# Kernel optimization log

Measured on AMD Instinct MI355X. Metric: run time of the kernel, lower is better.

## Reference

```python
import jax, jax.numpy as jnp
import numpy as np

N_NODES = 10000
N_EDGES = 100000
D_IN = 2 * 1280   # concat of row/col node embeddings
H1 = 512
H2 = 256


def gcn_conv(x, edge_index, W, b):
    """PyG GCNConv: add self-loops, symmetric deg^-1/2 normalization,
    x @ W then scatter-add of normalized messages, plus bias.
    num_nodes is inferred from x.shape[0] (here = n_edges, faithful to source)."""
    N = x.shape[0]
    loops = jnp.arange(N, dtype=edge_index.dtype)
    row = jnp.concatenate([edge_index[0], loops])  # sources
    col = jnp.concatenate([edge_index[1], loops])  # targets
    deg = jax.ops.segment_sum(jnp.ones_like(row, dtype=x.dtype), col, num_segments=N)
    dinv = jax.lax.rsqrt(deg)  # deg >= 1 thanks to self-loops
    norm = dinv[row] * dinv[col]  # [E+N]
    h = x @ W  # [N, out]
    out = jax.ops.segment_sum(h[row] * norm[:, None], col, num_segments=N)
    return out + b


def setup_inputs() -> dict:
    key = jax.random.key(0)
    ks = jax.random.split(key, 9)
    x = jax.random.normal(ks[0], (N_NODES, 1280), dtype=jnp.float32)
    edge_index = jax.random.randint(ks[1], (2, N_EDGES), 0, N_NODES, dtype=jnp.int32)
    # uniform noise for gumbel-sigmoid (torch.rand); keep strictly in (0,1)
    eps = jax.random.uniform(ks[2], (N_EDGES, 1), jnp.float32, 1e-6, 1.0 - 1e-6)
    W1 = jax.random.normal(ks[3], (D_IN, H1), jnp.float32) * (1.0 / np.sqrt(D_IN))
    b1 = jnp.zeros((H1,), jnp.float32)
    W2 = jax.random.normal(ks[4], (H1, H2), jnp.float32) * (1.0 / np.sqrt(H1))
    b2 = jnp.zeros((H2,), jnp.float32)
    Wl = jax.random.normal(ks[5], (H2, 1), jnp.float32) * (1.0 / np.sqrt(H2))
    bl = jnp.zeros((1,), jnp.float32)
    return {"x": x, "edge_index": edge_index, "eps": eps,
            "W1": W1, "b1": b1, "W2": W2, "b2": b2, "Wl": Wl, "bl": bl}


def reference(x, edge_index, eps, W1, b1, W2, b2, Wl, bl):
    rows, cols = edge_index[0], edge_index[1]
    # per-edge explainer input: concat of endpoint embeddings -> [E, 2560]
    input_embs = jnp.concatenate([x[rows], x[cols]], axis=1)
    h = jax.nn.relu(gcn_conv(input_embs, edge_index, W1, b1))
    h = jax.nn.relu(gcn_conv(h, edge_index, W2, b2))
    pre = h @ Wl + bl  # [E, 1] sampling weights
    # gumbel-sigmoid sampling (temperature = 1.0)
    gate = jnp.log(eps) - jnp.log1p(-eps) + pre
    mask = jax.nn.sigmoid(gate)
    pos, neg = mask, 1.0 - mask
    kld = jnp.mean(pos * jnp.log(pos / 0.5 + 1e-8) + neg * jnp.log(neg / 0.5 + 1e-9))
    return (kld, mask)
```

## Files before the change

kernel.cpp:

```cpp
#include <hip/hip_runtime.h>
#include <cstdint>
#include <cstddef>

#define H1DIM 512
#define H2DIM 256
#define DNODE 1280
#define NPACK 1024
#define APAD  40

typedef __attribute__((ext_vector_type(8))) short short8v;
typedef __attribute__((ext_vector_type(4))) float f32x4;
typedef __attribute__((ext_vector_type(4))) unsigned short us4;

__device__ __forceinline__ unsigned short f2bf(float f) {
    unsigned int u = __builtin_bit_cast(unsigned int, f);
    u += 0x7fffu + ((u >> 16) & 1u);
    return (unsigned short)(u >> 16);
}
__device__ __forceinline__ float bf2f(unsigned short h) {
    unsigned int u = ((unsigned int)h) << 16;
    return __builtin_bit_cast(float, u);
}

__global__ void hist_k(const int* __restrict__ e1, int* __restrict__ hist, int E) {
    int e = blockIdx.x * 256 + threadIdx.x;
    if (e < E) atomicAdd(&hist[e1[e]], 1);
}
__global__ __launch_bounds__(1024) void scan_dinv_k(
    const int* __restrict__ hist, int* __restrict__ off, int* __restrict__ cursor,
    float* __restrict__ dinv, int N)
{
    __shared__ int part[1024];
    const int t = threadIdx.x;
    const int per = (N + 1023) / 1024;
    const int base = t * per;
    int s = 0;
    for (int i = 0; i < per; ++i) { int b = base + i; if (b < N) s += hist[b]; }
    part[t] = s;
    __syncthreads();
    for (int d = 1; d < 1024; d <<= 1) {
        int v = (t >= d) ? part[t - d] : 0;
        __syncthreads();
        part[t] += v;
        __syncthreads();
    }
    int run = (t == 0) ? 0 : part[t - 1];
    for (int i = 0; i < per; ++i) {
        int b = base + i;
        if (b < N) {
            int h = hist[b];
            off[b] = run;
            run += h;
            cursor[b] = 0;
            dinv[b] = rsqrtf(1.0f + (float)h);
        }
    }
    if (t == 1023) off[N] = run;
}
__global__ void fill_k(const int* __restrict__ e0, const int* __restrict__ e1,
                       const int* __restrict__ off, int* __restrict__ cursor,
                       int* __restrict__ srcs, int E) {
    int e = blockIdx.x * 256 + threadIdx.x;
    if (e < E) {
        int t = e1[e];
        int p = off[t] + atomicAdd(&cursor[t], 1);
        srcs[p] = e0[e];
    }
}

__global__ void cvt_x_k(const float* __restrict__ src, unsigned short* __restrict__ dst, int n) {
    int i = blockIdx.x * 256 + threadIdx.x;
    if (i * 4 < n) {
        f32x4 v = *reinterpret_cast<const f32x4*>(src + (size_t)i * 4);
        us4 o;
        o[0] = f2bf(v.x); o[1] = f2bf(v.y); o[2] = f2bf(v.z); o[3] = f2bf(v.w);
        *reinterpret_cast<us4*>(dst + (size_t)i * 4) = o;
    }
}

__global__ __launch_bounds__(256) void transpose_cvt_k(
    const float* __restrict__ src, unsigned short* __restrict__ dst, int ldsrc, int lddst)
{
    __shared__ float tile[32][33];
    const int c0 = blockIdx.x * 32;
    const int r0 = blockIdx.y * 32;
    const int tx = threadIdx.x & 31;
    const int ty = threadIdx.x >> 5;
#pragma unroll
    for (int rr = ty; rr < 32; rr += 8)
        tile[rr][tx] = src[(size_t)(r0 + rr) * ldsrc + c0 + tx];
    __syncthreads();
#pragma unroll
    for (int rr = ty; rr < 32; rr += 8)
        dst[(size_t)(c0 + rr) * lddst + r0 + tx] = f2bf(tile[tx][rr]);
}

template <int MODE>
__global__ __launch_bounds__(512) void gemm_u_k(
    const unsigned short* __restrict__ Ab,
    const unsigned short* __restrict__ Bt,
    unsigned short* __restrict__ Cb,
    const unsigned short* __restrict__ out1b,
    const unsigned short* __restrict__ XWb16,
    const float* __restrict__ b1,
    const float* __restrict__ b2,
    const float* __restrict__ Wl,
    const int* __restrict__ e0, const int* __restrict__ e1,
    float* __restrict__ h2f, float* __restrict__ pre_raw,
    int M, int K, int Nn, int nwg)
{
    __shared__ unsigned short As[2][128 * APAD];
    __shared__ unsigned short Bs[2][256 * APAD];
    __shared__ float b1s[H1DIM];
    __shared__ float b2s[H2DIM];
    __shared__ float wls[H2DIM];
    __shared__ float preacc[128];

    const int tid  = threadIdx.x;
    const int lane = tid & 63;
    const int w    = tid >> 6;
    const int wm   = w >> 2, wn = w & 3;

    int mb, n0;
    if (MODE == 0) {
        const int q = nwg >> 3, r = nwg & 7;
        const int xcd = blockIdx.x & 7;
        const int base = (xcd < r) ? xcd * (q + 1) : r * (q + 1) + (xcd - r) * q;
        const int wg = base + (blockIdx.x >> 3);
        mb = wg >> 2;
        n0 = (wg & 3) << 8;
    } else {
        mb = blockIdx.x;
        n0 = 0;
    }
    const int m0 = mb * 128;

    if (MODE == 1) {
        if (tid < 128) preacc[tid] = 0.f;
        if (tid < 256) { b2s[tid] = b2[tid]; wls[tid] = Wl[tid]; }
        b1s[tid] = b1[tid];
    }

    const int sa_r = tid >> 2, sa_k = (tid & 3) << 3;
    const int sb_r = tid >> 1, sb_k = (tid & 1) << 4;
    const int gma  = m0 + sa_r;
    const bool aval = (gma < M);

    const unsigned short* bsrc = Bt + (size_t)(n0 + sb_r) * K + sb_k;
    const unsigned short* s1 = nullptr;
    const unsigned short* s2 = nullptr;
    bool dual = false;
    if (MODE == 0) {
        if (aval) s1 = Ab + (size_t)gma * K + sa_k;
    } else if (aval) {
        if (gma < Nn) {
            s1 = out1b + (size_t)gma * H1DIM + sa_k;
        } else {
            s1 = XWb16 + (size_t)e0[gma] * NPACK + sa_k;
            s2 = XWb16 + (size_t)e1[gma] * NPACK + H1DIM + sa_k;
            dual = true;
        }
    }
    if (MODE == 1) __syncthreads();

    f32x4 acc[4][4];
#pragma unroll
    for (int i = 0; i < 4; ++i)
#pragma unroll
        for (int j = 0; j < 4; ++j) acc[i][j] = f32x4{0.f, 0.f, 0.f, 0.f};

    short8v ab1, ab2, bb0, bb1;

    auto load_tile = [&](int k0) {
        bb0 = *reinterpret_cast<const short8v*>(bsrc + k0);
        bb1 = *reinterpret_cast<const short8v*>(bsrc + k0 + 8);
        if (aval) {
            ab1 = *reinterpret_cast<const short8v*>(s1 + k0);
            if (MODE == 1 && dual) ab2 = *reinterpret_cast<const short8v*>(s2 + k0);
        }
    };
    auto write_lds = [&](int buf, int k0) {
        *reinterpret_cast<short8v*>(&Bs[buf][sb_r * APAD + sb_k])     = bb0;
        *reinterpret_cast<short8v*>(&Bs[buf][sb_r * APAD + sb_k + 8]) = bb1;
        short8v av;
        if (!aval) {
            av = short8v{0,0,0,0,0,0,0,0};
        } else if (MODE == 0 || !dual) {
            av = ab1;
        } else {
#pragma unroll
            for (int ii = 0; ii < 8; ++ii) {
                float v = bf2f((unsigned short)ab1[ii]) + bf2f((unsigned short)ab2[ii])
                        + b1s[k0 + sa_k + ii];
                v = fmaxf(v, 0.f);
                av[ii] = (short)f2bf(v);
            }
        }
        *reinterpret_cast<short8v*>(&As[buf][sa_r * APAD + sa_k]) = av;
    };

    const int arow = wm * 64 + (lane & 15);
    const int brow = wn * 64 + (lane & 15);
    const int kq   = (lane >> 4) << 3;

    load_tile(0);
    int buf = 0;
    for (int k0 = 0; k0 < K; k0 += 32) {
        write_lds(buf, k0);
        __syncthreads();
        if (k0 + 32 < K) load_tile(k0 + 32);

        const unsigned short* as = As[buf];
        const unsigned short* bs = Bs[buf];
        short8v af[4], bfq[4];
#pragma unroll
        for (int i = 0; i < 4; ++i)
            af[i] = *reinterpret_cast<const short8v*>(&as[(arow + i * 16) * APAD + kq]);
#pragma unroll
        for (int j = 0; j < 4; ++j)
            bfq[j] = *reinterpret_cast<const short8v*>(&bs[(brow + j * 16) * APAD + kq]);
#pragma unroll
        for (int i = 0; i < 4; ++i)
#pragma unroll
            for (int j = 0; j < 4; ++j)
                acc[i][j] = __builtin_amdgcn_mfma_f32_16x16x32_bf16(af[i], bfq[j], acc[i][j], 0, 0, 0);
        buf ^= 1;
    }

    const int crow0 = m0 + wm * 64 + ((lane >> 4) << 2);
    if (MODE == 0) {
        const int ccol = n0 + wn * 64 + (lane & 15);
#pragma unroll
        for (int i = 0; i < 4; ++i)
#pragma unroll
            for (int q = 0; q < 4; ++q) {
                const int row = crow0 + i * 16 + q;
                if (row < M) {
#pragma unroll
                    for (int j = 0; j < 4; ++j)
                        Cb[(size_t)row * NPACK + ccol + j * 16] = f2bf(acc[i][j][q]);
                }
            }
    } else {
        const int cbase = wn * 64 + (lane & 15);
#pragma unroll
        for (int i = 0; i < 4; ++i)
#pragma unroll
            for (int q = 0; q < 4; ++q) {
                float v = 0.f;
#pragma unroll
                for (int j = 0; j < 4; ++j) {
                    const int c = cbase + j * 16;
                    v += fmaxf(acc[i][j][q] + b2s[c], 0.f) * wls[c];
                }
                v += __shfl_xor(v, 1, 64);
                v += __shfl_xor(v, 2, 64);
                v += __shfl_xor(v, 4, 64);
                v += __shfl_xor(v, 8, 64);
                if ((lane & 15) == 0)
                    atomicAdd(&preacc[wm * 64 + i * 16 + ((lane >> 4) << 2) + q], v);
            }
        if (m0 < Nn) {
            const int ccol = wn * 64 + (lane & 15);
#pragma unroll
            for (int i = 0; i < 4; ++i)
#pragma unroll
                for (int q = 0; q < 4; ++q) {
                    const int row = crow0 + i * 16 + q;
                    if (row < Nn) {
#pragma unroll
                        for (int j = 0; j < 4; ++j)
                            h2f[(size_t)row * H2DIM + ccol + j * 16] = acc[i][j][q];
                    }
                }
        }
        __syncthreads();
        if (tid < 128) {
            const int gm = m0 + tid;
            if (gm >= Nn && gm < M) pre_raw[gm] = preacc[tid];
        }
    }
}

__global__ __launch_bounds__(256) void build1_k(
    const unsigned short* __restrict__ XWb16, const float* __restrict__ dinv,
    const int* __restrict__ e0, const int* __restrict__ e1,
    float* __restrict__ H1s)
{
    const int r = blockIdx.x;
    const int a = e0[r], b = e1[r];
    const float dv = dinv[r];
    const unsigned short* pt = XWb16 + (size_t)a * NPACK;
    const unsigned short* pb = XWb16 + (size_t)b * NPACK + H1DIM;
    const int j = threadIdx.x * 2;
    const unsigned ut = *reinterpret_cast<const unsigned*>(pt + j);
    const unsigned ub = *reinterpret_cast<const unsigned*>(pb + j);
    float2 o;
    o.x = (bf2f((unsigned short)(ut & 0xffff)) + bf2f((unsigned short)(ub & 0xffff))) * dv;
    o.y = (bf2f((unsigned short)(ut >> 16))   + bf2f((unsigned short)(ub >> 16)))   * dv;
    *reinterpret_cast<float2*>(H1s + (size_t)r * H1DIM + j) = o;
}

__global__ __launch_bounds__(256) void agg1_k(
    const float* __restrict__ H1s, const int* __restrict__ off, const int* __restrict__ srcs,
    const float* __restrict__ b1, const float* __restrict__ dinv,
    unsigned short* __restrict__ out1b)
{
    const int t = blockIdx.x;
    const int j = threadIdx.x * 2;
    const int s0 = off[t], s1e = off[t + 1];
    const float dt = dinv[t];
    float2 acc = *reinterpret_cast<const float2*>(H1s + (size_t)t * H1DIM + j);
    for (int i = s0; i < s1e; ++i) {
        const float2 v = *reinterpret_cast<const float2*>(H1s + (size_t)srcs[i] * H1DIM + j);
        acc.x += v.x; acc.y += v.y;
    }
    const float ox = fmaxf(b1[j]     + dt * acc.x, 0.f);
    const float oy = fmaxf(b1[j + 1] + dt * acc.y, 0.f);
    const unsigned pk = (unsigned)f2bf(ox) | ((unsigned)f2bf(oy) << 16);
    *reinterpret_cast<unsigned*>(out1b + (size_t)t * H1DIM + j) = pk;
}

__global__ __launch_bounds__(256) void agg2_k(
    const float* __restrict__ h2f, const int* __restrict__ off, const int* __restrict__ srcs,
    const float* __restrict__ b2, const float* __restrict__ Wl,
    const float* __restrict__ dinv, float* __restrict__ pre_low)
{
    __shared__ float part[4];
    const int t = blockIdx.x;
    const int j = threadIdx.x;
    const int s0 = off[t], s1e = off[t + 1];
    const float dt = dinv[t];
    float acc = h2f[(size_t)t * H2DIM + j] * dt;
    for (int i = s0; i < s1e; ++i) {
        const int s = srcs[i];
        acc += h2f[(size_t)s * H2DIM + j] * dinv[s];
    }
    float p = fmaxf(b2[j] + dt * acc, 0.f) * Wl[j];
#pragma unroll
    for (int o = 32; o; o >>= 1) p += __shfl_down(p, o, 64);
    if ((j & 63) == 0) part[j >> 6] = p;
    __syncthreads();
    if (j == 0) pre_low[t] = part[0] + part[1] + part[2] + part[3];
}

__global__ __launch_bounds__(256) void final2_k(
    const float* __restrict__ pre_low, const float* __restrict__ pre_raw,
    const float* __restrict__ blp, const float* __restrict__ eps,
    float* __restrict__ dout, int E, int Nn)
{
    __shared__ float part[4];
    const int i = blockIdx.x * 256 + threadIdx.x;
    float kld = 0.f;
    if (i < E) {
        const float pre = ((i < Nn) ? pre_low[i] : pre_raw[i]) + blp[0];
        const float ee = eps[i];
        const float gate = logf(ee) - log1pf(-ee) + pre;
        const float m = 1.0f / (1.0f + expf(-gate));
        dout[1 + i] = m;
        const float pos = m, neg = 1.0f - m;
        kld = pos * logf(pos * 2.0f + 1e-8f) + neg * logf(neg * 2.0f + 1e-9f);
    }
#pragma unroll
    for (int o = 32; o; o >>= 1) kld += __shfl_down(kld, o, 64);
    const int lane = threadIdx.x & 63, wv = threadIdx.x >> 6;
    if (lane == 0) part[wv] = kld;
    __syncthreads();
    if (threadIdx.x == 0)
        atomicAdd(&dout[0], (part[0] + part[1] + part[2] + part[3]) / (float)E);
}

extern "C" void kernel_launch(void* const* d_in, const int* in_sizes, int n_in,
                              void* d_out, int out_size, void* d_ws, size_t ws_size,
                              hipStream_t stream)
{
    const float* x   = (const float*)d_in[0];
    const int*   ei  = (const int*)d_in[1];
    const float* eps = (const float*)d_in[2];
    const float* W1  = (const float*)d_in[3];
    const float* b1  = (const float*)d_in[4];
    const float* W2  = (const float*)d_in[5];
    const float* b2  = (const float*)d_in[6];
    const float* Wl  = (const float*)d_in[7];
    const float* bl  = (const float*)d_in[8];
    float* out = (float*)d_out;
    float* ws  = (float*)d_ws;

    const int N = in_sizes[0] / DNODE;
    const int E = in_sizes[1] / 2;
    const int* e0 = ei;
    const int* e1 = ei + E;

    float* dinv     = ws;
    float* H1s      = dinv + 16384;
    float* h2f      = H1s + (size_t)N * H1DIM;
    float* pre_raw  = h2f + (size_t)N * H2DIM;
    float* pre_low  = pre_raw + E;
    float* fend     = pre_low + 16384;
    unsigned short* XWb16 = (unsigned short*)fend;
    unsigned short* out1b = XWb16 + (size_t)N * NPACK;
    unsigned short* xb    = out1b + (size_t)N * H1DIM;
    unsigned short* Bpt1  = xb + (size_t)N * DNODE;
    unsigned short* W2t   = Bpt1 + (size_t)NPACK * DNODE;
    int* hist   = (int*)(W2t + (size_t)H2DIM * H1DIM);
    int* cursor = hist + N;
    int* off    = cursor + N;
    int* srcs   = off + (N + 1);

    hipMemsetAsync(hist, 0, (size_t)N * sizeof(int), stream);
    hipMemsetAsync(out, 0, sizeof(float), stream);

    hist_k<<<(E + 255) / 256, 256, 0, stream>>>(e1, hist, E);
    scan_dinv_k<<<1, 1024, 0, stream>>>(hist, off, cursor, dinv, N);
    fill_k<<<(E + 255) / 256, 256, 0, stream>>>(e0, e1, off, cursor, srcs, E);

    cvt_x_k<<<(N * DNODE / 4 + 255) / 256, 256, 0, stream>>>(x, xb, N * DNODE);
    transpose_cvt_k<<<dim3(H1DIM / 32, DNODE / 32), 256, 0, stream>>>(W1, Bpt1, H1DIM, DNODE);
    transpose_cvt_k<<<dim3(H1DIM / 32, DNODE / 32), 256, 0, stream>>>(
        W1 + (size_t)DNODE * H1DIM, Bpt1 + (size_t)H1DIM * DNODE, H1DIM, DNODE);
    transpose_cvt_k<<<dim3(H2DIM / 32, H1DIM / 32), 256, 0, stream>>>(W2, W2t, H2DIM, H1DIM);

    {
        const int nwg = 4 * ((N + 127) / 128);
        gemm_u_k<0><<<nwg, 512, 0, stream>>>(
            xb, Bpt1, XWb16, nullptr, nullptr, b1, b2, Wl, e0, e1,
            nullptr, nullptr, N, DNODE, 0, nwg);
    }

    build1_k<<<N, 256, 0, stream>>>(XWb16, dinv, e0, e1, H1s);
    agg1_k<<<N, 256, 0, stream>>>(H1s, off, srcs, b1, dinv, out1b);

    {
        const int nwg = (E + 127) / 128;
        gemm_u_k<1><<<nwg, 512, 0, stream>>>(
            nullptr, W2t, nullptr, out1b, XWb16, b1, b2, Wl, e0, e1,
            h2f, pre_raw, E, H1DIM, N, nwg);
    }

    agg2_k<<<N, 256, 0, stream>>>(h2f, off, srcs, b2, Wl, dinv, pre_low);

    final2_k<<<(E + 255) / 256, 256, 0, stream>>>(pre_low, pre_raw, bl, eps, out, E, N);
}
```

Baseline: 234.9 us.

## Halve GEMM M-tile to 64 rows and trim LDS to raise occupancy

Shrinks the GEMM block tile from 128 to 64 rows. Each wave now holds 2x4 MFMA accumulators instead of 4x4, and only half the threads stage A into LDS. The launch bounds now request 4 waves per EU, the b1 bias is kept in LDS as bf16, and b2/Wl are read into registers instead of LDS. The aim is more resident workgroups and more blocks for latency hiding. The cost is lower data reuse per block, since B is reloaded twice as often, plus a slight change in numerics from rounding b1 to bf16.

```diff
diff --git a/kernel.cpp b/kernel.cpp
--- a/kernel.cpp
+++ b/kernel.cpp
@@ -7,6 +7,7 @@
 #define DNODE 1280
 #define NPACK 1024
 #define APAD  40
+#define BM    64
 
 typedef __attribute__((ext_vector_type(8))) short short8v;
 typedef __attribute__((ext_vector_type(4))) float f32x4;
@@ -96,7 +97,7 @@
 }
 
 template <int MODE>
-__global__ __launch_bounds__(512) void gemm_u_k(
+__global__ __launch_bounds__(512, 4) void gemm_u_k(
     const unsigned short* __restrict__ Ab,
     const unsigned short* __restrict__ Bt,
     unsigned short* __restrict__ Cb,
@@ -109,12 +110,10 @@
     float* __restrict__ h2f, float* __restrict__ pre_raw,
     int M, int K, int Nn, int nwg)
 {
-    __shared__ unsigned short As[2][128 * APAD];
+    __shared__ unsigned short As[2][BM * APAD];
     __shared__ unsigned short Bs[2][256 * APAD];
-    __shared__ float b1s[H1DIM];
-    __shared__ float b2s[H2DIM];
-    __shared__ float wls[H2DIM];
-    __shared__ float preacc[128];
+    __shared__ unsigned short b1h[H1DIM];
+    __shared__ float preacc[BM];
 
     const int tid  = threadIdx.x;
     const int lane = tid & 63;
@@ -133,18 +132,18 @@
         mb = blockIdx.x;
         n0 = 0;
     }
-    const int m0 = mb * 128;
+    const int m0 = mb * BM;
 
     if (MODE == 1) {
-        if (tid < 128) preacc[tid] = 0.f;
-        if (tid < 256) { b2s[tid] = b2[tid]; wls[tid] = Wl[tid]; }
-        b1s[tid] = b1[tid];
-    }
-
+        if (tid < BM) preacc[tid] = 0.f;
+        b1h[tid] = f2bf(b1[tid]);
+    }
+
+    const bool astage = tid < 256;
     const int sa_r = tid >> 2, sa_k = (tid & 3) << 3;
     const int sb_r = tid >> 1, sb_k = (tid & 1) << 4;
     const int gma  = m0 + sa_r;
-    const bool aval = (gma < M);
+    const bool aval = astage && (gma < M);
 
     const unsigned short* bsrc = Bt + (size_t)(n0 + sb_r) * K + sb_k;
     const unsigned short* s1 = nullptr;
@@ -163,9 +162,9 @@
     }
     if (MODE == 1) __syncthreads();
 
-    f32x4 acc[4][4];
-#pragma unroll
-    for (int i = 0; i < 4; ++i)
+    f32x4 acc[2][4];
+#pragma unroll
+    for (int i = 0; i < 2; ++i)
 #pragma unroll
         for (int j = 0; j < 4; ++j) acc[i][j] = f32x4{0.f, 0.f, 0.f, 0.f};
 
@@ -182,24 +181,26 @@
     auto write_lds = [&](int buf, int k0) {
         *reinterpret_cast<short8v*>(&Bs[buf][sb_r * APAD + sb_k])     = bb0;
         *reinterpret_cast<short8v*>(&Bs[buf][sb_r * APAD + sb_k + 8]) = bb1;
-        short8v av;
-        if (!aval) {
-            av = short8v{0,0,0,0,0,0,0,0};
-        } else if (MODE == 0 || !dual) {
-            av = ab1;
-        } else {
-#pragma unroll
-            for (int ii = 0; ii < 8; ++ii) {
-                float v = bf2f((unsigned short)ab1[ii]) + bf2f((unsigned short)ab2[ii])
-                        + b1s[k0 + sa_k + ii];
-                v = fmaxf(v, 0.f);
-                av[ii] = (short)f2bf(v);
+        if (astage) {
+            short8v av;
+            if (!aval) {
+                av = short8v{0,0,0,0,0,0,0,0};
+            } else if (MODE == 0 || !dual) {
+                av = ab1;
+            } else {
+#pragma unroll
+                for (int ii = 0; ii < 8; ++ii) {
+                    float v = bf2f((unsigned short)ab1[ii]) + bf2f((unsigned short)ab2[ii])
+                            + bf2f(b1h[k0 + sa_k + ii]);
+                    v = fmaxf(v, 0.f);
+                    av[ii] = (short)f2bf(v);
+                }
             }
-        }
-        *reinterpret_cast<short8v*>(&As[buf][sa_r * APAD + sa_k]) = av;
+            *reinterpret_cast<short8v*>(&As[buf][sa_r * APAD + sa_k]) = av;
+        }
     };
 
-    const int arow = wm * 64 + (lane & 15);
+    const int arow = wm * 32 + (lane & 15);
     const int brow = wn * 64 + (lane & 15);
     const int kq   = (lane >> 4) << 3;
 
@@ -212,26 +213,26 @@
 
         const unsigned short* as = As[buf];
         const unsigned short* bs = Bs[buf];
-        short8v af[4], bfq[4];
-#pragma unroll
-        for (int i = 0; i < 4; ++i)
+        short8v af[2], bfq[4];
+#pragma unroll
+        for (int i = 0; i < 2; ++i)
             af[i] = *reinterpret_cast<const short8v*>(&as[(arow + i * 16) * APAD + kq]);
 #pragma unroll
         for (int j = 0; j < 4; ++j)
             bfq[j] = *reinterpret_cast<const short8v*>(&bs[(brow + j * 16) * APAD + kq]);
 #pragma unroll
-        for (int i = 0; i < 4; ++i)
+        for (int i = 0; i < 2; ++i)
 #pragma unroll
             for (int j = 0; j < 4; ++j)
                 acc[i][j] = __builtin_amdgcn_mfma_f32_16x16x32_bf16(af[i], bfq[j], acc[i][j], 0, 0, 0);
         buf ^= 1;
     }
 
-    const int crow0 = m0 + wm * 64 + ((lane >> 4) << 2);
+    const int crow0 = m0 + wm * 32 + ((lane >> 4) << 2);
     if (MODE == 0) {
         const int ccol = n0 + wn * 64 + (lane & 15);
 #pragma unroll
-        for (int i = 0; i < 4; ++i)
+        for (int i = 0; i < 2; ++i)
 #pragma unroll
             for (int q = 0; q < 4; ++q) {
                 const int row = crow0 + i * 16 + q;
@@ -243,27 +244,28 @@
             }
     } else {
         const int cbase = wn * 64 + (lane & 15);
-#pragma unroll
-        for (int i = 0; i < 4; ++i)
+        float b2v[4], wlv[4];
+#pragma unroll
+        for (int j = 0; j < 4; ++j) { b2v[j] = b2[cbase + j * 16]; wlv[j] = Wl[cbase + j * 16]; }
+#pragma unroll
+        for (int i = 0; i < 2; ++i)
 #pragma unroll
             for (int q = 0; q < 4; ++q) {
                 float v = 0.f;
 #pragma unroll
-                for (int j = 0; j < 4; ++j) {
-                    const int c = cbase + j * 16;
-                    v += fmaxf(acc[i][j][q] + b2s[c], 0.f) * wls[c];
-                }
+                for (int j = 0; j < 4; ++j)
+                    v += fmaxf(acc[i][j][q] + b2v[j], 0.f) * wlv[j];
                 v += __shfl_xor(v, 1, 64);
                 v += __shfl_xor(v, 2, 64);
                 v += __shfl_xor(v, 4, 64);
                 v += __shfl_xor(v, 8, 64);
                 if ((lane & 15) == 0)
-                    atomicAdd(&preacc[wm * 64 + i * 16 + ((lane >> 4) << 2) + q], v);
+                    atomicAdd(&preacc[wm * 32 + i * 16 + ((lane >> 4) << 2) + q], v);
             }
         if (m0 < Nn) {
             const int ccol = wn * 64 + (lane & 15);
 #pragma unroll
-            for (int i = 0; i < 4; ++i)
+            for (int i = 0; i < 2; ++i)
 #pragma unroll
                 for (int q = 0; q < 4; ++q) {
                     const int row = crow0 + i * 16 + q;
@@ -275,7 +277,7 @@
                 }
         }
         __syncthreads();
-        if (tid < 128) {
+        if (tid < BM) {
             const int gm = m0 + tid;
             if (gm >= Nn && gm < M) pre_raw[gm] = preacc[tid];
         }
@@ -421,7 +423,7 @@
     transpose_cvt_k<<<dim3(H2DIM / 32, H1DIM / 32), 256, 0, stream>>>(W2, W2t, H2DIM, H1DIM);
 
     {
-        const int nwg = 4 * ((N + 127) / 128);
+        const int nwg = 4 * ((N + BM - 1) / BM);
         gemm_u_k<0><<<nwg, 512, 0, stream>>>(
             xb, Bpt1, XWb16, nullptr, nullptr, b1, b2, Wl, e0, e1,
             nullptr, nullptr, N, DNODE, 0, nwg);
@@ -431,7 +433,7 @@
     agg1_k<<<N, 256, 0, stream>>>(H1s, off, srcs, b1, dinv, out1b);
 
     {
-        const int nwg = (E + 127) / 128;
+        const int nwg = (E + BM - 1) / BM;
         gemm_u_k<1><<<nwg, 512, 0, stream>>>(
             nullptr, W2t, nullptr, out1b, XWb16, b1, b2, Wl, e0, e1,
             h2f, pre_raw, E, H1DIM, N, nwg);
```

Result: slower. 257.3 us (+9.6%).
